# Kernel optimization log

Measured on AMD Instinct MI355X. Metric: run time of the kernel, lower is better.

The kernel has to match this reference:

```python
import jax, jax.numpy as jnp
import numpy as np

B, T, A, F_IN = 32, 128, 22, 32
H1, C1 = 4, 128  # heads, gnn_hidden_dim
NEG_SLOPE = 0.2  # GATConv default leaky_relu slope


def setup_inputs() -> dict:
    key = jax.random.key(0)
    ks = jax.random.split(key, 12)
    g = lambda k, shape: jax.random.normal(k, shape, dtype=jnp.float32) * 0.05
    d1 = H1 * C1  # 512, concat output dim of multi-head layers
    return {
        "features": jax.random.normal(ks[0], (B, T, A, F_IN), dtype=jnp.float32),
        "W1": g(ks[1], (F_IN, H1, C1)), "as1": g(ks[2], (H1, C1)), "ad1": g(ks[3], (H1, C1)), "b1": jnp.zeros((d1,), jnp.float32),
        "W2": g(ks[4], (d1, H1, C1)), "as2": g(ks[5], (H1, C1)), "ad2": g(ks[6], (H1, C1)), "b2": jnp.zeros((d1,), jnp.float32),
        "W3": g(ks[7], (d1, 1, C1)), "as3": g(ks[8], (1, C1)), "ad3": g(ks[9], (1, C1)), "b3": jnp.zeros((C1,), jnp.float32),
        "Wc": g(ks[10], (C1, 1)), "bc": jnp.zeros((1,), jnp.float32),
    }


def _gat(x, W, a_src, a_dst, b, concat):
    # x: [G, A, F]; complete graph + self loops == dense attention over all A nodes.
    h = jnp.einsum('gaf,fhc->gahc', x, W)           # [G, A, H, C]
    s = jnp.einsum('gahc,hc->gha', h, a_src)        # att_src . h_j
    d = jnp.einsum('gahc,hc->gha', h, a_dst)        # att_dst . h_i
    logits = d[:, :, :, None] + s[:, :, None, :]    # [G, H, i, j] edge j->i
    logits = jnp.where(logits >= 0, logits, NEG_SLOPE * logits)
    alpha = jax.nn.softmax(logits, axis=-1)         # softmax over source nodes j
    out = jnp.einsum('ghij,gjhc->gihc', alpha, h)   # [G, A, H, C]
    G_, A_, H_, C_ = out.shape
    out = out.reshape(G_, A_, H_ * C_) if concat else out.mean(axis=2)
    return out + b


def reference(features, W1, as1, ad1, b1, W2, as2, ad2, b2, W3, as3, ad3, b3, Wc, bc):
    Bb, Tt, Aa, Ff = features.shape
    x = features.reshape(Bb * Tt, Aa, Ff)           # [G, A, F], G = B*T frame-graphs
    x = jax.nn.relu(_gat(x, W1, as1, ad1, b1, True))
    x = jax.nn.relu(_gat(x, W2, as2, ad2, b2, True))
    x = jax.nn.relu(_gat(x, W3, as3, ad3, b3, False))
    pooled = x.mean(axis=1)                         # global_mean_pool over 22 agents
    return (pooled @ Wc + bc)[:, 0]                 # [G] logits
```

## Files before the change

### kernel.cpp

```cpp
#include <hip/hip_runtime.h>

typedef unsigned short u16;
typedef unsigned int   u32;
typedef unsigned long long u64;
typedef short bf16x8 __attribute__((ext_vector_type(8)));
typedef float f32x4  __attribute__((ext_vector_type(4)));
typedef u32   u32x4  __attribute__((ext_vector_type(4)));

#define NA 22
#define FIN 32
#define XS_STR 520
#define AL_STR 24

#define W1_OFF 0
#define W2_OFF 16384
#define W3_OFF 278528
#define E1_OFF 344064
#define E2_OFF 344576
#define E3_OFF 352768
#define WS_TOTAL 360960

__device__ u16 f2b(float f) {
    unsigned int x = __float_as_uint(f);
    x = (x + 0x7fffu + ((x >> 16) & 1u)) >> 16;
    return (u16)x;
}

__device__ __forceinline__ u32 cvtpk(float lo, float hi) {
    u32 r;
    asm("v_cvt_pk_bf16_f32 %0, %1, %2" : "=v"(r) : "v"(lo), "v"(hi));
    return r;
}

__device__ __forceinline__ u32 dpp_swap1(u32 v) {
    return (u32)__builtin_amdgcn_mov_dpp((int)v, 0xB1, 0xF, 0xF, true);
}

__device__ __forceinline__ u32 pair_merge(u32 own, u32 nb, int par) {
    return par ? ((nb >> 16) | (own & 0xffff0000u))
               : ((own & 0xffffu) | (nb << 16));
}

__global__ void swizzle_kernel(const float* W1, const float* W2, const float* W3, u16* ws)
{
    int t = blockIdx.x * 256 + threadIdx.x;
    const float* W; int NT, nshift, base, loc;
    if (t < W2_OFF)      { W = W1; NT = 32; nshift = 9; base = W1_OFF; loc = t; }
    else if (t < W3_OFF) { W = W2; NT = 32; nshift = 9; base = W2_OFF; loc = t - W2_OFF; }
    else if (t < E1_OFF) { W = W3; NT = 8;  nshift = 7; base = W3_OFF; loc = t - W3_OFF; }
    else { return; }
    int k = loc >> nshift;
    int n = loc & ((1 << nshift) - 1);
    u16 v = f2b(W[loc]);
    int kt = k >> 5, quad = (k & 31) >> 3, j = k & 7;
    int nt = n >> 4, lm = n & 15;
    int lane = (quad << 4) | lm;
    ws[base + (((kt * NT + nt) << 9) | (lane << 3) | j)] = v;
}

__global__ void wav_kernel(const float* W1, const float* as1, const float* ad1,
                           const float* W2, const float* as2, const float* ad2,
                           const float* W3, const float* as3, const float* ad3,
                           u16* ws)
{
    int wid = blockIdx.x * 4 + (threadIdx.x >> 6);
    int lane = threadIdx.x & 63;
    int grp = lane >> 4, c4 = lane & 15;

    if (wid < 544) {
        const float* W; const float* asp; const float* adp; int k, base;
        if (wid < 32) { W = W1; asp = as1; adp = ad1; k = wid;      base = E1_OFF; }
        else          { W = W2; asp = as2; adp = ad2; k = wid - 32; base = E2_OFF; }
        int h = grp;
        const float4* wp = (const float4*)(W + k * 512 + lane * 8);
        float4 wa = wp[0], wb = wp[1];
        const float4* sp = (const float4*)(asp + h * 128 + c4 * 8);
        const float4* dp = (const float4*)(adp + h * 128 + c4 * 8);
        float4 sa = sp[0], sb = sp[1];
        float4 da = dp[0], db = dp[1];
        float ps = wa.x*sa.x + wa.y*sa.y + wa.z*sa.z + wa.w*sa.w
                 + wb.x*sb.x + wb.y*sb.y + wb.z*sb.z + wb.w*sb.w;
        float pd = wa.x*da.x + wa.y*da.y + wa.z*da.z + wa.w*da.w
                 + wb.x*db.x + wb.y*db.y + wb.z*db.z + wb.w*db.w;
        #pragma unroll
        for (int off = 1; off <= 8; off <<= 1) {
            ps += __shfl_xor(ps, off);
            pd += __shfl_xor(pd, off);
        }
        int kt = k >> 5, quad = (k & 31) >> 3, j = k & 7;
        if (c4 < 4) {
            int col = c4 * 4 + h;
            float v = (c4 == 0) ? ps : (c4 == 1) ? pd : 0.0f;
            ws[base + (kt << 9) + (((quad << 4) | col) << 3) + j] = f2b(v);
        }
    } else if (wid < 672) {
        int k = (wid - 544) * 4 + grp;
        const float4* wp = (const float4*)(W3 + k * 128 + c4 * 8);
        float4 wa = wp[0], wb = wp[1];
        const float4* sp = (const float4*)(as3 + c4 * 8);
        const float4* dp = (const float4*)(ad3 + c4 * 8);
        float4 sa = sp[0], sb = sp[1];
        float4 da = dp[0], db = dp[1];
        float ps = wa.x*sa.x + wa.y*sa.y + wa.z*sa.z + wa.w*sa.w
                 + wb.x*sb.x + wb.y*sb.y + wb.z*sb.z + wb.w*sb.w;
        float pd = wa.x*da.x + wa.y*da.y + wa.z*da.z + wa.w*da.w
                 + wb.x*db.x + wb.y*db.y + wb.z*db.z + wb.w*db.w;
        #pragma unroll
        for (int off = 1; off <= 8; off <<= 1) {
            ps += __shfl_xor(ps, off);
            pd += __shfl_xor(pd, off);
        }
        int kt = k >> 5, quad = (k & 31) >> 3, j = k & 7;
        float v = (c4 == 0) ? ps : (c4 == 1) ? pd : 0.0f;
        ws[E3_OFF + (kt << 9) + (((quad << 4) | c4) << 3) + j] = f2b(v);
    }
}

__device__ __forceinline__ void softmax_al(const float* sw, u16* al_slot, int lane)
{
    if (lane < NA) {
        float di = sw[24 + lane];
        f32x4 c0 = *(const f32x4*)(sw);
        f32x4 c1 = *(const f32x4*)(sw + 4);
        f32x4 c2 = *(const f32x4*)(sw + 8);
        f32x4 c3 = *(const f32x4*)(sw + 12);
        f32x4 c4 = *(const f32x4*)(sw + 16);
        float s20 = sw[20], s21 = sw[21];
        float lg[NA];
        float mx = -1.0e30f, ss = 0.0f;
        #pragma unroll
        for (int j = 0; j < NA; ++j) {
            float sj = (j < 4)  ? c0[j]      : (j < 8)  ? c1[j - 4]  :
                       (j < 12) ? c2[j - 8]  : (j < 16) ? c3[j - 12] :
                       (j < 20) ? c4[j - 16] : (j == 20) ? s20 : s21;
            float l = di + sj;
            l = fmaxf(l, 0.2f * l);
            lg[j] = l;
            mx = fmaxf(mx, l);
        }
        #pragma unroll
        for (int j = 0; j < NA; ++j) {
            float e = __expf(lg[j] - mx);
            lg[j] = e;
            ss += e;
        }
        float inv = 1.0f / ss;
        u32 pk[12];
        #pragma unroll
        for (int j2 = 0; j2 < 11; ++j2) {
            pk[j2] = cvtpk(lg[2 * j2] * inv, lg[2 * j2 + 1] * inv);
        }
        pk[11] = 0;
        u32* arow = (u32*)(al_slot + lane * AL_STR);
        *(u32x4*)(arow)     = (u32x4){pk[0], pk[1], pk[2],  pk[3]};
        *(u32x4*)(arow + 4) = (u32x4){pk[4], pk[5], pk[6],  pk[7]};
        *(u32x4*)(arow + 8) = (u32x4){pk[8], pk[9], pk[10], pk[11]};
    }
}

__device__ __forceinline__ void store_sd(float* swp, f32x4 e0, f32x4 e1, int quad)
{
    *(f32x4*)(swp + quad * 4) = e0;
    if (quad == 0) { *(f32x4*)(swp + 16) = e1; }
    else if (quad == 1) { swp[20] = e1[0]; swp[21] = e1[1]; }
}

template<int KT, int NT, int NTW, int H>
__device__ __forceinline__ void gat_layer(
    const u16* Wsw, const u16* Wext, const float* bias,
    u16* xs, float* svw, u16* al)
{
    int tid  = threadIdx.x;
    int wave = tid >> 6, lane = tid & 63;
    int quad = lane >> 4, lm = lane & 15;
    int par  = lane & 1;
    int r1 = 16 + lm; if (r1 >= NA) { r1 = lm; }

    f32x4 acc0[NTW], acc1[NTW], accE0, accE1;

    {
        const u16* a0base = xs + lm * XS_STR + quad * 8;
        const u16* a1base = xs + r1 * XS_STR + quad * 8;
        const u16* wbase  = Wsw + ((wave * NTW) << 9) + (lane << 3);
        const u16* ebase  = Wext + (lane << 3);

        f32x4 z4 = {0.f, 0.f, 0.f, 0.f};
        #pragma unroll
        for (int n = 0; n < NTW; ++n) { acc0[n] = z4; acc1[n] = z4; }
        accE0 = z4; accE1 = z4;

        bf16x8 bbuf[2][NTW], ebuf[2], ab0[2], ab1[2];
        #pragma unroll
        for (int n = 0; n < NTW; ++n) { bbuf[0][n] = *(const bf16x8*)(wbase + (n << 9)); }
        ebuf[0] = *(const bf16x8*)(ebase);
        ab0[0] = *(const bf16x8*)(a0base);
        ab1[0] = *(const bf16x8*)(a1base);

        #pragma unroll
        for (int kt = 0; kt < KT; ++kt) {
            const int cur = kt & 1;
            const int nxt = cur ^ 1;
            if (kt + 1 < KT) {
                const u16* wn = wbase + (((kt + 1) * NT) << 9);
                #pragma unroll
                for (int n = 0; n < NTW; ++n) { bbuf[nxt][n] = *(const bf16x8*)(wn + (n << 9)); }
                ebuf[nxt] = *(const bf16x8*)(ebase + ((kt + 1) << 9));
                ab0[nxt] = *(const bf16x8*)(a0base + (kt + 1) * 32);
                ab1[nxt] = *(const bf16x8*)(a1base + (kt + 1) * 32);
            }
            #pragma unroll
            for (int n = 0; n < NTW; ++n) {
                acc0[n] = __builtin_amdgcn_mfma_f32_16x16x32_bf16(ab0[cur], bbuf[cur][n], acc0[n], 0, 0, 0);
                acc1[n] = __builtin_amdgcn_mfma_f32_16x16x32_bf16(ab1[cur], bbuf[cur][n], acc1[n], 0, 0, 0);
            }
            accE0 = __builtin_amdgcn_mfma_f32_16x16x32_bf16(ab0[cur], ebuf[cur], accE0, 0, 0, 0);
            accE1 = __builtin_amdgcn_mfma_f32_16x16x32_bf16(ab1[cur], ebuf[cur], accE1, 0, 0, 0);
        }
    }

    int head = (H == 4) ? (wave >> 1) : 0;
    float* sw = svw + wave * 48;
    if (lm == head)     { store_sd(sw,      accE0, accE1, quad); }
    if (lm == head + H) { store_sd(sw + 24, accE0, accE1, quad); }

    bf16x8 bfrag[NTW];
    {
        int s0 = (((quad & 1) << 5) | lm) << 2;
        int s2 = s0 + 64;
        bool hi = (quad >= 2);
        #pragma unroll
        for (int n = 0; n < NTW; ++n) {
            u32 P0a = cvtpk(acc0[n][0], acc0[n][1]);
            u32 P1a = cvtpk(acc0[n][2], acc0[n][3]);
            u32 P0b = cvtpk(acc1[n][0], acc1[n][1]);
            u32 P1b = cvtpk(acc1[n][2], acc1[n][3]);
            u32 w0a = (u32)__builtin_amdgcn_ds_bpermute(s0, (int)P0a);
            u32 w0b = (u32)__builtin_amdgcn_ds_bpermute(s0, (int)P0b);
            u32 w1a = (u32)__builtin_amdgcn_ds_bpermute(s0, (int)P1a);
            u32 w1b = (u32)__builtin_amdgcn_ds_bpermute(s0, (int)P1b);
            u32 w2a = (u32)__builtin_amdgcn_ds_bpermute(s2, (int)P0a);
            u32 w2b = (u32)__builtin_amdgcn_ds_bpermute(s2, (int)P0b);
            u32 w3a = (u32)__builtin_amdgcn_ds_bpermute(s2, (int)P1a);
            union { u32 w[4]; bf16x8 v; } bu;
            bu.w[0] = hi ? w0b : w0a;
            bu.w[1] = hi ? w1b : w1a;
            bu.w[2] = hi ? w2b : w2a;
            bu.w[3] = hi ? 0u  : w3a;
            bfrag[n] = bu.v;
        }
    }

    softmax_al(sw, al + wave * NA * AL_STR, lane);

    const u16* albase = al + wave * NA * AL_STR;
    bf16x8 zb = {0, 0, 0, 0, 0, 0, 0, 0};
    bf16x8 pa0 = (quad < 3) ? *(const bf16x8*)(albase + lm * AL_STR + quad * 8) : zb;
    bf16x8 pa1 = (quad < 3) ? *(const bf16x8*)(albase + r1 * AL_STR + quad * 8) : zb;

    f32x4 agg0[NTW], agg1[NTW];
    f32x4 z4 = {0.f, 0.f, 0.f, 0.f};
    float bv[NTW];
    #pragma unroll
    for (int n = 0; n < NTW; ++n) {
        int col = (wave * NTW + n) * 16 + lm;
        bv[n] = bias[col];
        agg0[n] = __builtin_amdgcn_mfma_f32_16x16x32_bf16(pa0, bfrag[n], z4, 0, 0, 0);
        agg1[n] = __builtin_amdgcn_mfma_f32_16x16x32_bf16(pa1, bfrag[n], z4, 0, 0, 0);
    }

    __syncthreads();

    #pragma unroll
    for (int n = 0; n < NTW; ++n) {
        int col = (wave * NTW + n) * 16 + lm;
        int cold = col & ~1;
        float v0 = fmaxf(agg0[n][0] + bv[n], 0.0f);
        float v1 = fmaxf(agg0[n][1] + bv[n], 0.0f);
        float v2 = fmaxf(agg0[n][2] + bv[n], 0.0f);
        float v3 = fmaxf(agg0[n][3] + bv[n], 0.0f);
        u32 wa0 = cvtpk(v0, v1), wa1 = cvtpk(v2, v3);
        u32 nb0 = dpp_swap1(wa0), nb1 = dpp_swap1(wa1);
        u32 d0 = pair_merge(wa0, nb0, par);
        u32 d1 = pair_merge(wa1, nb1, par);
        *(u32*)(xs + (quad * 4 + par) * XS_STR + cold)     = d0;
        *(u32*)(xs + (quad * 4 + 2 + par) * XS_STR + cold) = d1;
        if (quad < 2) {
            float u0 = fmaxf(agg1[n][0] + bv[n], 0.0f);
            float u1 = fmaxf(agg1[n][1] + bv[n], 0.0f);
            u32 wb0 = cvtpk(u0, u1);
            u32 nbb = dpp_swap1(wb0);
            *(u32*)(xs + (16 + quad * 4 + par) * XS_STR + cold) = pair_merge(wb0, nbb, par);
            if (quad == 0) {
                float u2 = fmaxf(agg1[n][2] + bv[n], 0.0f);
                float u3 = fmaxf(agg1[n][3] + bv[n], 0.0f);
                u32 wb1 = cvtpk(u2, u3);
                u32 nbc = dpp_swap1(wb1);
                *(u32*)(xs + (18 + par) * XS_STR + cold) = pair_merge(wb1, nbc, par);
            }
        }
    }
    __syncthreads();
}

template<int KT, int NT>
__device__ __forceinline__ void gat_final(
    const u16* Wsw, const u16* Wext, const float* bias,
    const u16* xs, float* svw, u16* al,
    const float* Wc, const float* bc, float* partial, float* out, int g)
{
    int tid  = threadIdx.x;
    int wave = tid >> 6, lane = tid & 63;
    int quad = lane >> 4, lm = lane & 15;
    int r1 = 16 + lm; if (r1 >= NA) { r1 = lm; }

    f32x4 acc0, acc1, accE0, accE1;

    {
        const u16* a0base = xs + lm * XS_STR + quad * 8;
        const u16* a1base = xs + r1 * XS_STR + quad * 8;
        const u16* wbase  = Wsw + (wave << 9) + (lane << 3);
        const u16* ebase  = Wext + (lane << 3);

        f32x4 z4 = {0.f, 0.f, 0.f, 0.f};
        acc0 = z4; acc1 = z4; accE0 = z4; accE1 = z4;

        bf16x8 bbuf[2], ebuf[2], ab0[2], ab1[2];
        bbuf[0] = *(const bf16x8*)(wbase);
        ebuf[0] = *(const bf16x8*)(ebase);
        ab0[0] = *(const bf16x8*)(a0base);
        ab1[0] = *(const bf16x8*)(a1base);

        #pragma unroll
        for (int kt = 0; kt < KT; ++kt) {
            const int cur = kt & 1;
            const int nxt = cur ^ 1;
            if (kt + 1 < KT) {
                bbuf[nxt] = *(const bf16x8*)(wbase + (((kt + 1) * NT) << 9));
                ebuf[nxt] = *(const bf16x8*)(ebase + ((kt + 1) << 9));
                ab0[nxt] = *(const bf16x8*)(a0base + (kt + 1) * 32);
                ab1[nxt] = *(const bf16x8*)(a1base + (kt + 1) * 32);
            }
            acc0  = __builtin_amdgcn_mfma_f32_16x16x32_bf16(ab0[cur], bbuf[cur], acc0, 0, 0, 0);
            acc1  = __builtin_amdgcn_mfma_f32_16x16x32_bf16(ab1[cur], bbuf[cur], acc1, 0, 0, 0);
            accE0 = __builtin_amdgcn_mfma_f32_16x16x32_bf16(ab0[cur], ebuf[cur], accE0, 0, 0, 0);
            accE1 = __builtin_amdgcn_mfma_f32_16x16x32_bf16(ab1[cur], ebuf[cur], accE1, 0, 0, 0);
        }
    }

    float* sw = svw + wave * 48;
    if (lm == 0) { store_sd(sw,      accE0, accE1, quad); }
    if (lm == 1) { store_sd(sw + 24, accE0, accE1, quad); }

    bf16x8 bfrag;
    {
        int s0 = (((quad & 1) << 5) | lm) << 2;
        int s2 = s0 + 64;
        bool hi = (quad >= 2);
        u32 P0a = cvtpk(acc0[0], acc0[1]);
        u32 P1a = cvtpk(acc0[2], acc0[3]);
        u32 P0b = cvtpk(acc1[0], acc1[1]);
        u32 P1b = cvtpk(acc1[2], acc1[3]);
        u32 w0a = (u32)__builtin_amdgcn_ds_bpermute(s0, (int)P0a);
        u32 w0b = (u32)__builtin_amdgcn_ds_bpermute(s0, (int)P0b);
        u32 w1a = (u32)__builtin_amdgcn_ds_bpermute(s0, (int)P1a);
        u32 w1b = (u32)__builtin_amdgcn_ds_bpermute(s0, (int)P1b);
        u32 w2a = (u32)__builtin_amdgcn_ds_bpermute(s2, (int)P0a);
        u32 w2b = (u32)__builtin_amdgcn_ds_bpermute(s2, (int)P0b);
        u32 w3a = (u32)__builtin_amdgcn_ds_bpermute(s2, (int)P1a);
        union { u32 w[4]; bf16x8 v; } bu;
        bu.w[0] = hi ? w0b : w0a;
        bu.w[1] = hi ? w1b : w1a;
        bu.w[2] = hi ? w2b : w2a;
        bu.w[3] = hi ? 0u  : w3a;
        bfrag = bu.v;
    }

    softmax_al(sw, al + wave * NA * AL_STR, lane);

    const u16* albase = al + wave * NA * AL_STR;
    bf16x8 zb = {0, 0, 0, 0, 0, 0, 0, 0};
    bf16x8 pa0 = (quad < 3) ? *(const bf16x8*)(albase + lm * AL_STR + quad * 8) : zb;
    bf16x8 pa1 = (quad < 3) ? *(const bf16x8*)(albase + r1 * AL_STR + quad * 8) : zb;

    f32x4 z4 = {0.f, 0.f, 0.f, 0.f};
    f32x4 agg0 = __builtin_amdgcn_mfma_f32_16x16x32_bf16(pa0, bfrag, z4, 0, 0, 0);
    f32x4 agg1 = __builtin_amdgcn_mfma_f32_16x16x32_bf16(pa1, bfrag, z4, 0, 0, 0);

    int col = wave * 16 + lm;
    float bvv = bias[col];
    float cs = 0.0f;
    #pragma unroll
    for (int r = 0; r < 4; ++r) { cs += fmaxf(agg0[r] + bvv, 0.0f); }
    #pragma unroll
    for (int r = 0; r < 4; ++r) {
        int row1 = 16 + quad * 4 + r;
        if (row1 < NA) { cs += fmaxf(agg1[r] + bvv, 0.0f); }
    }
    cs += __shfl_xor(cs, 16);
    cs += __shfl_xor(cs, 32);
    float part = (cs / 22.0f) * Wc[col];
    part += __shfl_xor(part, 1);
    part += __shfl_xor(part, 2);
    part += __shfl_xor(part, 4);
    part += __shfl_xor(part, 8);
    if (lane == 0) { partial[wave] = part; }
    __syncthreads();
    if (tid == 0) {
        float t = 0.0f;
        #pragma unroll
        for (int w = 0; w < 8; ++w) { t += partial[w]; }
        out[g] = t + bc[0];
    }
}

__global__ void __launch_bounds__(512, 3)
pressgnn_kernel(const float* feats, const u16* ws,
                const float* b1, const float* b2, const float* b3,
                const float* Wc, const float* bc,
                float* out)
{
    __shared__ __align__(16) u16 xs[NA * XS_STR];
    __shared__ __align__(16) u16 al[8 * NA * AL_STR];
    __shared__ __align__(16) float svw[8 * 48];
    __shared__ float partial[8];

    int g = blockIdx.x;
    int tid = threadIdx.x;

    for (int i = tid; i < NA * FIN / 2; i += 512) {
        float2 v = *(const float2*)(feats + g * NA * FIN + i * 2);
        int row = (i * 2) >> 5;
        int c   = (i * 2) & 31;
        *(u32*)(xs + row * XS_STR + c) = cvtpk(v.x, v.y);
    }
    __syncthreads();

    gat_layer<1,  32, 4, 4>(ws + W1_OFF, ws + E1_OFF, b1, xs, svw, al);
    gat_layer<16, 32, 4, 4>(ws + W2_OFF, ws + E2_OFF, b2, xs, svw, al);
    gat_final<16, 8>(ws + W3_OFF, ws + E3_OFF, b3, xs, svw, al,
                     Wc, bc, partial, out, g);
}

extern "C" void kernel_launch(void* const* d_in, const int* in_sizes, int n_in,
                              void* d_out, int out_size, void* d_ws, size_t ws_size,
                              hipStream_t stream) {
    const float* feats = (const float*)d_in[0];
    const float* W1  = (const float*)d_in[1];
    const float* as1 = (const float*)d_in[2];
    const float* ad1 = (const float*)d_in[3];
    const float* b1  = (const float*)d_in[4];
    const float* W2  = (const float*)d_in[5];
    const float* as2 = (const float*)d_in[6];
    const float* ad2 = (const float*)d_in[7];
    const float* b2  = (const float*)d_in[8];
    const float* W3  = (const float*)d_in[9];
    const float* as3 = (const float*)d_in[10];
    const float* ad3 = (const float*)d_in[11];
    const float* b3  = (const float*)d_in[12];
    const float* Wc  = (const float*)d_in[13];
    const float* bc  = (const float*)d_in[14];
    float* out = (float*)d_out;
    u16* ws = (u16*)d_ws;

    swizzle_kernel<<<dim3(1344), dim3(256), 0, stream>>>(W1, W2, W3, ws);
    wav_kernel<<<dim3(168), dim3(256), 0, stream>>>(W1, as1, ad1, W2, as2, ad2,
                                                    W3, as3, ad3, ws);

    pressgnn_kernel<<<dim3(out_size), dim3(512), 0, stream>>>(
        feats, ws, b1, b2, b3, Wc, bc, out);
}
```

Measured before the change: 255.4 us.

## Compute attention logits once per head and share softmax via LDS

```diff
diff --git a/kernel.cpp b/kernel.cpp
--- a/kernel.cpp
+++ b/kernel.cpp
@@ -30,15 +30,6 @@
     u32 r;
     asm("v_cvt_pk_bf16_f32 %0, %1, %2" : "=v"(r) : "v"(lo), "v"(hi));
     return r;
-}
-
-__device__ __forceinline__ u32 dpp_swap1(u32 v) {
-    return (u32)__builtin_amdgcn_mov_dpp((int)v, 0xB1, 0xF, 0xF, true);
-}
-
-__device__ __forceinline__ u32 pair_merge(u32 own, u32 nb, int par) {
-    return par ? ((nb >> 16) | (own & 0xffff0000u))
-               : ((own & 0xffffu) | (nb << 16));
 }
 
 __global__ void swizzle_kernel(const float* W1, const float* W2, const float* W3, u16* ws)
@@ -173,8 +164,9 @@
     int tid  = threadIdx.x;
     int wave = tid >> 6, lane = tid & 63;
     int quad = lane >> 4, lm = lane & 15;
-    int par  = lane & 1;
     int r1 = 16 + lm; if (r1 >= NA) { r1 = lm; }
+    int head = (H == 4) ? (wave >> 1) : 0;
+    bool doE = (H == 4) ? ((wave & 1) == 0) : (wave == 0);
 
     f32x4 acc0[NTW], acc1[NTW], accE0, accE1;
 
@@ -189,39 +181,51 @@
         for (int n = 0; n < NTW; ++n) { acc0[n] = z4; acc1[n] = z4; }
         accE0 = z4; accE1 = z4;
 
-        bf16x8 bbuf[2][NTW], ebuf[2], ab0[2], ab1[2];
+        bf16x8 bbuf[3][NTW], ebuf[2], ab0[2], ab1[2];
         #pragma unroll
         for (int n = 0; n < NTW; ++n) { bbuf[0][n] = *(const bf16x8*)(wbase + (n << 9)); }
-        ebuf[0] = *(const bf16x8*)(ebase);
+        if (KT > 1) {
+            #pragma unroll
+            for (int n = 0; n < NTW; ++n) { bbuf[1][n] = *(const bf16x8*)(wbase + ((NT + n) << 9)); }
+        }
+        if (doE) { ebuf[0] = *(const bf16x8*)(ebase); }
         ab0[0] = *(const bf16x8*)(a0base);
         ab1[0] = *(const bf16x8*)(a1base);
 
         #pragma unroll
         for (int kt = 0; kt < KT; ++kt) {
-            const int cur = kt & 1;
-            const int nxt = cur ^ 1;
+            const int c3 = kt % 3;
+            const int cA = kt & 1;
+            const int nA = cA ^ 1;
+            if (kt + 2 < KT) {
+                const int p3 = (kt + 2) % 3;
+                const u16* wn = wbase + (((kt + 2) * NT) << 9);
+                #pragma unroll
+                for (int n = 0; n < NTW; ++n) { bbuf[p3][n] = *(const bf16x8*)(wn + (n << 9)); }
+            }
             if (kt + 1 < KT) {
-                const u16* wn = wbase + (((kt + 1) * NT) << 9);
-                #pragma unroll
-                for (int n = 0; n < NTW; ++n) { bbuf[nxt][n] = *(const bf16x8*)(wn + (n << 9)); }
-                ebuf[nxt] = *(const bf16x8*)(ebase + ((kt + 1) << 9));
-                ab0[nxt] = *(const bf16x8*)(a0base + (kt + 1) * 32);
-                ab1[nxt] = *(const bf16x8*)(a1base + (kt + 1) * 32);
+                if (doE) { ebuf[nA] = *(const bf16x8*)(ebase + ((kt + 1) << 9)); }
+                ab0[nA] = *(const bf16x8*)(a0base + (kt + 1) * 32);
+                ab1[nA] = *(const bf16x8*)(a1base + (kt + 1) * 32);
             }
             #pragma unroll
             for (int n = 0; n < NTW; ++n) {
-                acc0[n] = __builtin_amdgcn_mfma_f32_16x16x32_bf16(ab0[cur], bbuf[cur][n], acc0[n], 0, 0, 0);
-                acc1[n] = __builtin_amdgcn_mfma_f32_16x16x32_bf16(ab1[cur], bbuf[cur][n], acc1[n], 0, 0, 0);
-            }
-            accE0 = __builtin_amdgcn_mfma_f32_16x16x32_bf16(ab0[cur], ebuf[cur], accE0, 0, 0, 0);
-            accE1 = __builtin_amdgcn_mfma_f32_16x16x32_bf16(ab1[cur], ebuf[cur], accE1, 0, 0, 0);
-        }
-    }
-
-    int head = (H == 4) ? (wave >> 1) : 0;
-    float* sw = svw + wave * 48;
-    if (lm == head)     { store_sd(sw,      accE0, accE1, quad); }
-    if (lm == head + H) { store_sd(sw + 24, accE0, accE1, quad); }
+                acc0[n] = __builtin_amdgcn_mfma_f32_16x16x32_bf16(ab0[cA], bbuf[c3][n], acc0[n], 0, 0, 0);
+                acc1[n] = __builtin_amdgcn_mfma_f32_16x16x32_bf16(ab1[cA], bbuf[c3][n], acc1[n], 0, 0, 0);
+            }
+            if (doE) {
+                accE0 = __builtin_amdgcn_mfma_f32_16x16x32_bf16(ab0[cA], ebuf[cA], accE0, 0, 0, 0);
+                accE1 = __builtin_amdgcn_mfma_f32_16x16x32_bf16(ab1[cA], ebuf[cA], accE1, 0, 0, 0);
+            }
+        }
+    }
+
+    float* sw = svw + head * 48;
+    if (doE) {
+        if (lm == head)     { store_sd(sw,      accE0, accE1, quad); }
+        if (lm == head + H) { store_sd(sw + 24, accE0, accE1, quad); }
+        softmax_al(sw, al + head * NA * AL_STR, lane);
+    }
 
     bf16x8 bfrag[NTW];
     {
@@ -250,9 +254,9 @@
         }
     }
 
-    softmax_al(sw, al + wave * NA * AL_STR, lane);
-
-    const u16* albase = al + wave * NA * AL_STR;
+    __syncthreads();
+
+    const u16* albase = al + head * NA * AL_STR;
     bf16x8 zb = {0, 0, 0, 0, 0, 0, 0, 0};
     bf16x8 pa0 = (quad < 3) ? *(const bf16x8*)(albase + lm * AL_STR + quad * 8) : zb;
     bf16x8 pa1 = (quad < 3) ? *(const bf16x8*)(albase + r1 * AL_STR + quad * 8) : zb;
@@ -268,34 +272,33 @@
         agg1[n] = __builtin_amdgcn_mfma_f32_16x16x32_bf16(pa1, bfrag[n], z4, 0, 0, 0);
     }
 
-    __syncthreads();
-
     #pragma unroll
     for (int n = 0; n < NTW; ++n) {
         int col = (wave * NTW + n) * 16 + lm;
-        int cold = col & ~1;
+        u16* cbase = xs + col;
         float v0 = fmaxf(agg0[n][0] + bv[n], 0.0f);
         float v1 = fmaxf(agg0[n][1] + bv[n], 0.0f);
         float v2 = fmaxf(agg0[n][2] + bv[n], 0.0f);
         float v3 = fmaxf(agg0[n][3] + bv[n], 0.0f);
         u32 wa0 = cvtpk(v0, v1), wa1 = cvtpk(v2, v3);
-        u32 nb0 = dpp_swap1(wa0), nb1 = dpp_swap1(wa1);
-        u32 d0 = pair_merge(wa0, nb0, par);
-        u32 d1 = pair_merge(wa1, nb1, par);
-        *(u32*)(xs + (quad * 4 + par) * XS_STR + cold)     = d0;
-        *(u32*)(xs + (quad * 4 + 2 + par) * XS_STR + cold) = d1;
+        int r0 = quad * 4;
+        cbase[(r0 + 0) * XS_STR] = (u16)wa0;
+        cbase[(r0 + 1) * XS_STR] = (u16)(wa0 >> 16);
+        cbase[(r0 + 2) * XS_STR] = (u16)wa1;
+        cbase[(r0 + 3) * XS_STR] = (u16)(wa1 >> 16);
         if (quad < 2) {
             float u0 = fmaxf(agg1[n][0] + bv[n], 0.0f);
             float u1 = fmaxf(agg1[n][1] + bv[n], 0.0f);
             u32 wb0 = cvtpk(u0, u1);
-            u32 nbb = dpp_swap1(wb0);
-            *(u32*)(xs + (16 + quad * 4 + par) * XS_STR + cold) = pair_merge(wb0, nbb, par);
+            int r16 = 16 + quad * 4;
+            cbase[(r16 + 0) * XS_STR] = (u16)wb0;
+            cbase[(r16 + 1) * XS_STR] = (u16)(wb0 >> 16);
             if (quad == 0) {
                 float u2 = fmaxf(agg1[n][2] + bv[n], 0.0f);
                 float u3 = fmaxf(agg1[n][3] + bv[n], 0.0f);
                 u32 wb1 = cvtpk(u2, u3);
-                u32 nbc = dpp_swap1(wb1);
-                *(u32*)(xs + (18 + par) * XS_STR + cold) = pair_merge(wb1, nbc, par);
+                cbase[18 * XS_STR] = (u16)wb1;
+                cbase[19 * XS_STR] = (u16)(wb1 >> 16);
             }
         }
     }
@@ -312,6 +315,7 @@
     int wave = tid >> 6, lane = tid & 63;
     int quad = lane >> 4, lm = lane & 15;
     int r1 = 16 + lm; if (r1 >= NA) { r1 = lm; }
+    bool doE = (wave == 0);
 
     f32x4 acc0, acc1, accE0, accE1;
 
@@ -324,32 +328,41 @@
         f32x4 z4 = {0.f, 0.f, 0.f, 0.f};
         acc0 = z4; acc1 = z4; accE0 = z4; accE1 = z4;
 
-        bf16x8 bbuf[2], ebuf[2], ab0[2], ab1[2];
+        bf16x8 bbuf[3], ebuf[2], ab0[2], ab1[2];
         bbuf[0] = *(const bf16x8*)(wbase);
-        ebuf[0] = *(const bf16x8*)(ebase);
+        if (KT > 1) { bbuf[1] = *(const bf16x8*)(wbase + (NT << 9)); }
+        if (doE) { ebuf[0] = *(const bf16x8*)(ebase); }
         ab0[0] = *(const bf16x8*)(a0base);
         ab1[0] = *(const bf16x8*)(a1base);
 
         #pragma unroll
         for (int kt = 0; kt < KT; ++kt) {
-            const int cur = kt & 1;
-            const int nxt = cur ^ 1;
+            const int c3 = kt % 3;
+            const int cA = kt & 1;
+            const int nA = cA ^ 1;
+            if (kt + 2 < KT) {
+                bbuf[(kt + 2) % 3] = *(const bf16x8*)(wbase + (((kt + 2) * NT) << 9));
+            }
             if (kt + 1 < KT) {
-                bbuf[nxt] = *(const bf16x8*)(wbase + (((kt + 1) * NT) << 9));
-                ebuf[nxt] = *(const bf16x8*)(ebase + ((kt + 1) << 9));
-                ab0[nxt] = *(const bf16x8*)(a0base + (kt + 1) * 32);
-                ab1[nxt] = *(const bf16x8*)(a1base + (kt + 1) * 32);
-            }
-            acc0  = __builtin_amdgcn_mfma_f32_16x16x32_bf16(ab0[cur], bbuf[cur], acc0, 0, 0, 0);
-            acc1  = __builtin_amdgcn_mfma_f32_16x16x32_bf16(ab1[cur], bbuf[cur], acc1, 0, 0, 0);
-            accE0 = __builtin_amdgcn_mfma_f32_16x16x32_bf16(ab0[cur], ebuf[cur], accE0, 0, 0, 0);
-            accE1 = __builtin_amdgcn_mfma_f32_16x16x32_bf16(ab1[cur], ebuf[cur], accE1, 0, 0, 0);
-        }
-    }
-
-    float* sw = svw + wave * 48;
-    if (lm == 0) { store_sd(sw,      accE0, accE1, quad); }
-    if (lm == 1) { store_sd(sw + 24, accE0, accE1, quad); }
+                if (doE) { ebuf[nA] = *(const bf16x8*)(ebase + ((kt + 1) << 9)); }
+                ab0[nA] = *(const bf16x8*)(a0base + (kt + 1) * 32);
+                ab1[nA] = *(const bf16x8*)(a1base + (kt + 1) * 32);
+            }
+            acc0 = __builtin_amdgcn_mfma_f32_16x16x32_bf16(ab0[cA], bbuf[c3], acc0, 0, 0, 0);
+            acc1 = __builtin_amdgcn_mfma_f32_16x16x32_bf16(ab1[cA], bbuf[c3], acc1, 0, 0, 0);
+            if (doE) {
+                accE0 = __builtin_amdgcn_mfma_f32_16x16x32_bf16(ab0[cA], ebuf[cA], accE0, 0, 0, 0);
+                accE1 = __builtin_amdgcn_mfma_f32_16x16x32_bf16(ab1[cA], ebuf[cA], accE1, 0, 0, 0);
+            }
+        }
+    }
+
+    float* sw = svw;
+    if (doE) {
+        if (lm == 0) { store_sd(sw,      accE0, accE1, quad); }
+        if (lm == 1) { store_sd(sw + 24, accE0, accE1, quad); }
+        softmax_al(sw, al, lane);
+    }
 
     bf16x8 bfrag;
     {
@@ -375,12 +388,11 @@
         bfrag = bu.v;
     }
 
-    softmax_al(sw, al + wave * NA * AL_STR, lane);
-
-    const u16* albase = al + wave * NA * AL_STR;
+    __syncthreads();
+
     bf16x8 zb = {0, 0, 0, 0, 0, 0, 0, 0};
-    bf16x8 pa0 = (quad < 3) ? *(const bf16x8*)(albase + lm * AL_STR + quad * 8) : zb;
-    bf16x8 pa1 = (quad < 3) ? *(const bf16x8*)(albase + r1 * AL_STR + quad * 8) : zb;
+    bf16x8 pa0 = (quad < 3) ? *(const bf16x8*)(al + lm * AL_STR + quad * 8) : zb;
+    bf16x8 pa1 = (quad < 3) ? *(const bf16x8*)(al + r1 * AL_STR + quad * 8) : zb;
 
     f32x4 z4 = {0.f, 0.f, 0.f, 0.f};
     f32x4 agg0 = __builtin_amdgcn_mfma_f32_16x16x32_bf16(pa0, bfrag, z4, 0, 0, 0);
@@ -420,8 +432,8 @@
                 float* out)
 {
     __shared__ __align__(16) u16 xs[NA * XS_STR];
-    __shared__ __align__(16) u16 al[8 * NA * AL_STR];
-    __shared__ __align__(16) float svw[8 * 48];
+    __shared__ __align__(16) u16 al[4 * NA * AL_STR];
+    __shared__ __align__(16) float svw[4 * 48];
     __shared__ float partial[8];
 
     int g = blockIdx.x;
```

New measurement: 296.6 us. +16.1%, slower.
